# Performance work log

Hardware: AMD Instinct MI355X
Metric: run time of the kernel (lower is better)

Reference implementation:

```python
import jax, jax.numpy as jnp
import numpy as np

IMG_DIM = 512
BATCH = 32


def setup_inputs() -> dict:
    key = jax.random.key(0)
    k1, k2, k3, k4, k5 = jax.random.split(key, 5)
    N, D = BATCH, IMG_DIM
    return {
        "im1": jax.random.normal(k1, (N, 3, D, D), jnp.float32),
        "im2": jax.random.normal(k2, (N, 3, D, D), jnp.float32),
        "C": jax.random.normal(k3, (N, 2, D, D), jnp.float32),
        "M1": jax.random.uniform(k4, (N, 1, D, D), jnp.float32),
        "M2": jax.random.uniform(k5, (N, 1, D, D), jnp.float32),
    }


def _grid_q(D):
    # q[0] = row coord repeated, q[1] = col coord tiled -> [2, D*D]
    x = jnp.arange(D, dtype=jnp.float32)
    return jnp.stack([jnp.repeat(x, D), jnp.tile(x, D)], axis=0)


def _get_pixel(qi, nb_x, nb_y, imflat, D):
    # qi: [N,2,HW]; nb_x, nb_y: [N,HW] integer-valued floats; imflat: [N,3,HW]
    w = (1.0 - jnp.abs(qi[:, 0] - nb_x)) * (1.0 - jnp.abs(qi[:, 1] - nb_y))  # [N,HW]
    inds = (nb_y + D * nb_x).astype(jnp.int32)  # ind = y + D*x, detached from grads
    inds = jax.lax.stop_gradient(inds)
    px = jnp.take_along_axis(imflat, inds[:, None, :], axis=2)  # [N,3,HW]
    return w[:, None, :] * px


def _masked_rp(image, mask, qi_orig, D):
    N = image.shape[0]
    HW = D * D
    imflat = image.reshape(N, 3, HW)
    qi = jnp.clip(qi_orig, 0.001, D - 1.001)  # [N,2,HW]
    fx, fy = jnp.floor(qi[:, 0]), jnp.floor(qi[:, 1])
    cx, cy = jnp.ceil(qi[:, 0]), jnp.ceil(qi[:, 1])
    res = (_get_pixel(qi, fx, fy, imflat, D)
           + _get_pixel(qi, cx, fy, imflat, D)
           + _get_pixel(qi, fx, cy, imflat, D)
           + _get_pixel(qi, cx, cy, imflat, D))  # [N,3,HW]
    oob_loss = jnp.mean((qi_orig - qi) ** 2) / (D * D) * 0.01
    res_img = res.reshape(image.shape)
    return res_img * mask, oob_loss


def _forward(im1, im2, C, M1, M2):
    N = im1.shape[0]
    D = im1.shape[2]
    q = _grid_q(D)[None]  # [1,2,HW]
    Cflat = C.reshape(N, 2, D * D)
    a, la = _masked_rp(im1, M1, q + Cflat, D)
    b, lb = _masked_rp(im2, M2, q - Cflat, D)
    return a + b, la + lb


def reference(im1, im2, C, M1, M2):
    return _forward(im1, im2, C, M1, M2)
```

## Files before the change

kernel.cpp:

```cpp
#include <hip/hip_runtime.h>


constexpr int D    = 512;
constexpr int HW   = D * D;
constexpr int NB   = 32;
constexpr int NPIX = NB * HW;
constexpr float LOSS_SCALE = (float)(0.01 / (2.0 * (double)NPIX * (double)HW));

__device__ __forceinline__ float3 sample3(const float* __restrict__ p,
                                          float q0o, float q1o,
                                          float& oob, float& wscale)
{
    const float hi = 510.999f;
    float q0 = fminf(fmaxf(q0o, 0.001f), hi);
    float q1 = fminf(fmaxf(q1o, 0.001f), hi);
    float d0 = q0o - q0, d1 = q1o - q1;
    oob = fmaf(d0, d0, oob);
    oob = fmaf(d1, d1, oob);

    float fx = floorf(q0), fy = floorf(q1);
    float ax = q0 - fx,    ay = q1 - fy;
    wscale = ((ax == 0.0f) ? 2.0f : 1.0f) * ((ay == 0.0f) ? 2.0f : 1.0f);

    int off = (int)fy + (((int)fx) << 9);

    float r[3];
    #pragma unroll
    for (int c = 0; c < 3; ++c) {
        const float* pc = p + c * HW;
        float v00 = pc[off];
        float v01 = pc[off + 1];
        float v10 = pc[off + 512];
        float v11 = pc[off + 513];
        float top = fmaf(ay, v01 - v00, v00);
        float bot = fmaf(ay, v11 - v10, v10);
        r[c] = fmaf(ax, bot - top, top);
    }
    return make_float3(r[0], r[1], r[2]);
}

__global__ void __launch_bounds__(256)
vm_fwd(const float* __restrict__ im1, const float* __restrict__ im2,
       const float* __restrict__ C,   const float* __restrict__ M1,
       const float* __restrict__ M2,  float* __restrict__ out)
{
    const int b    = blockIdx.x;
    const int slab = ((b & 7) << 10) | (b >> 3);

    const int n   = slab >> 8;
    const int hw0 = ((slab & 255) << 10) | threadIdx.x;

    const float* Cn = C   + (size_t)n * 2 * HW;
    const float* Mp = M1  + (size_t)n * HW;
    const float* Mq = M2  + (size_t)n * HW;
    const float* p1 = im1 + (size_t)n * 3 * HW;
    const float* p2 = im2 + (size_t)n * 3 * HW;
    float* op       = out + (size_t)n * 3 * HW;

    float oob = 0.0f;

    #pragma unroll
    for (int j = 0; j < 4; ++j) {
        const int hw = hw0 + j * 256;
        const float qx = (float)(hw >> 9);
        const float qy = (float)(hw & 511);

        float c0 = __builtin_nontemporal_load(Cn + hw);
        float c1 = __builtin_nontemporal_load(Cn + HW + hw);
        float m1 = __builtin_nontemporal_load(Mp + hw);
        float m2 = __builtin_nontemporal_load(Mq + hw);

        float sA, sB;
        float3 av = sample3(p1, qx + c0, qy + c1, oob, sA);
        float3 bv = sample3(p2, qx - c0, qy - c1, oob, sB);
        float w1 = m1 * sA;
        float w2 = m2 * sB;

        __builtin_nontemporal_store(fmaf(av.x, w1, bv.x * w2), op + hw);
        __builtin_nontemporal_store(fmaf(av.y, w1, bv.y * w2), op + HW + hw);
        __builtin_nontemporal_store(fmaf(av.z, w1, bv.z * w2), op + 2 * HW + hw);
    }

    #pragma unroll
    for (int off = 32; off > 0; off >>= 1)
        oob += __shfl_down(oob, off, 64);

    __shared__ float wave_sums[4];
    int lane = threadIdx.x & 63;
    int wave = threadIdx.x >> 6;
    if (lane == 0) wave_sums[wave] = oob;
    __syncthreads();
    if (threadIdx.x == 0) {
        float s = wave_sums[0] + wave_sums[1] + wave_sums[2] + wave_sums[3];
        atomicAdd(out + (size_t)3 * NPIX, s * LOSS_SCALE);
    }
}

extern "C" void kernel_launch(void* const* d_in, const int* in_sizes, int n_in,
                              void* d_out, int out_size, void* d_ws, size_t ws_size,
                              hipStream_t stream) {
    const float* im1 = (const float*)d_in[0];
    const float* im2 = (const float*)d_in[1];
    const float* C   = (const float*)d_in[2];
    const float* M1  = (const float*)d_in[3];
    const float* M2  = (const float*)d_in[4];
    float* out = (float*)d_out;

    hipMemsetAsync(out + (size_t)3 * NPIX, 0, sizeof(float), stream);

    vm_fwd<<<8192, 256, 0, stream>>>(im1, im2, C, M1, M2, out);
}
```

Baseline: 371.8 us.

## Stage an eight-row image window in LDS for bilinear gathers

Each block copies an 8-row, 3-channel window of each source image into shared memory with vectorised loads. It then serves the bilinear gathers from LDS, falling back to global memory when a displaced sample lands outside the window. The flow and mask loads are hoisted ahead of the two image passes, and im1 and im2 are processed one after the other. The goal is to replace scattered global gathers with LDS reads, at the cost of a 48KB LDS footprint that limits occupancy, about 4x redundant window reads per block, and extra barriers.

```diff
diff --git a/kernel.cpp b/kernel.cpp
--- a/kernel.cpp
+++ b/kernel.cpp
@@ -7,9 +7,22 @@
 constexpr int NPIX = NB * HW;
 constexpr float LOSS_SCALE = (float)(0.01 / (2.0 * (double)NPIX * (double)HW));
 
-__device__ __forceinline__ float3 sample3(const float* __restrict__ p,
-                                          float q0o, float q1o,
-                                          float& oob, float& wscale)
+typedef float f4 __attribute__((ext_vector_type(4)));
+
+constexpr int WROWS = 8;
+constexpr int LDSZ  = 3 * WROWS * 512;
+
+__device__ __forceinline__ float lerp2(float v00, float v01, float v10, float v11,
+                                       float ax, float ay)
+{
+    float top = fmaf(ay, v01 - v00, v00);
+    float bot = fmaf(ay, v11 - v10, v10);
+    return fmaf(ax, bot - top, top);
+}
+
+struct Coord { float ax, ay, sc; int off; int u; bool in; };
+
+__device__ __forceinline__ Coord make_coord(float q0o, float q1o, int wlo, float& oob)
 {
     const float hi = 510.999f;
     float q0 = fminf(fmaxf(q0o, 0.001f), hi);
@@ -19,24 +32,56 @@
     oob = fmaf(d1, d1, oob);
 
     float fx = floorf(q0), fy = floorf(q1);
-    float ax = q0 - fx,    ay = q1 - fy;
-    wscale = ((ax == 0.0f) ? 2.0f : 1.0f) * ((ay == 0.0f) ? 2.0f : 1.0f);
+    Coord c;
+    c.ax = q0 - fx;
+    c.ay = q1 - fy;
+    c.sc = ((c.ax == 0.0f) ? 2.0f : 1.0f) * ((c.ay == 0.0f) ? 2.0f : 1.0f);
+    int ix = (int)fx, iy = (int)fy;
+    c.off = iy + (ix << 9);
+    c.u   = ix - wlo;
+    c.in  = (unsigned)c.u <= (unsigned)(WROWS - 2);
+    return c;
+}
 
-    int off = (int)fy + (((int)fx) << 9);
+__device__ __forceinline__ float3 sample_win(const float* __restrict__ lds,
+                                             const float* __restrict__ p,
+                                             const Coord& c)
+{
+    float r0, r1, r2;
+    if (c.in) {
+        int base = (c.u << 9) + (c.off & 511);
+        float a00 = lds[base],        a01 = lds[base + 1];
+        float a10 = lds[base + 512],  a11 = lds[base + 513];
+        r0 = lerp2(a00, a01, a10, a11, c.ax, c.ay);
+        float b00 = lds[base + 4096], b01 = lds[base + 4097];
+        float b10 = lds[base + 4608], b11 = lds[base + 4609];
+        r1 = lerp2(b00, b01, b10, b11, c.ax, c.ay);
+        float c00 = lds[base + 8192], c01 = lds[base + 8193];
+        float c10 = lds[base + 8704], c11 = lds[base + 8705];
+        r2 = lerp2(c00, c01, c10, c11, c.ax, c.ay);
+    } else {
+        const float* pc = p + c.off;
+        r0 = lerp2(pc[0],        pc[1],        pc[512],        pc[513],        c.ax, c.ay);
+        r1 = lerp2(pc[HW],       pc[HW + 1],   pc[HW + 512],   pc[HW + 513],   c.ax, c.ay);
+        r2 = lerp2(pc[2 * HW],   pc[2*HW + 1], pc[2*HW + 512], pc[2*HW + 513], c.ax, c.ay);
+    }
+    return make_float3(r0, r1, r2);
+}
 
-    float r[3];
+__device__ __forceinline__ void stage(float* __restrict__ lds,
+                                      const float* __restrict__ img,
+                                      int wlo, int tid)
+{
     #pragma unroll
-    for (int c = 0; c < 3; ++c) {
-        const float* pc = p + c * HW;
-        float v00 = pc[off];
-        float v01 = pc[off + 1];
-        float v10 = pc[off + 512];
-        float v11 = pc[off + 513];
-        float top = fmaf(ay, v01 - v00, v00);
-        float bot = fmaf(ay, v11 - v10, v10);
-        r[c] = fmaf(ax, bot - top, top);
+    for (int q = 0; q < 12; ++q) {
+        int e4    = q * 256 + tid;
+        int plane = e4 >> 7;
+        int ch    = plane >> 3;
+        int u     = plane & 7;
+        int col   = (e4 & 127) << 2;
+        f4 v = *(const f4*)(img + (size_t)ch * HW + ((wlo + u) << 9) + col);
+        *(f4*)(lds + (plane << 9) + col) = v;
     }
-    return make_float3(r[0], r[1], r[2]);
 }
 
 __global__ void __launch_bounds__(256)
@@ -44,11 +89,17 @@
        const float* __restrict__ C,   const float* __restrict__ M1,
        const float* __restrict__ M2,  float* __restrict__ out)
 {
+    __shared__ float lds[LDSZ];
+
     const int b    = blockIdx.x;
     const int slab = ((b & 7) << 10) | (b >> 3);
 
     const int n   = slab >> 8;
-    const int hw0 = ((slab & 255) << 10) | threadIdx.x;
+    const int k   = slab & 255;
+    const int r   = k << 1;
+    const int tid = threadIdx.x;
+    const int hw0 = (k << 10) | tid;
+    const int wlo = min(max(r - 3, 0), D - WROWS);
 
     const float* Cn = C   + (size_t)n * 2 * HW;
     const float* Mp = M1  + (size_t)n * HW;
@@ -57,28 +108,44 @@
     const float* p2 = im2 + (size_t)n * 3 * HW;
     float* op       = out + (size_t)n * 3 * HW;
 
+    float c0v[4], c1v[4], m1v[4], m2v[4];
+    #pragma unroll
+    for (int j = 0; j < 4; ++j) {
+        int hw = hw0 + j * 256;
+        c0v[j] = __builtin_nontemporal_load(Cn + hw);
+        c1v[j] = __builtin_nontemporal_load(Cn + HW + hw);
+        m1v[j] = __builtin_nontemporal_load(Mp + hw);
+        m2v[j] = __builtin_nontemporal_load(Mq + hw);
+    }
+
     float oob = 0.0f;
 
+    stage(lds, p1, wlo, tid);
+    __syncthreads();
+    float a0[4], a1[4], a2[4];
     #pragma unroll
     for (int j = 0; j < 4; ++j) {
-        const int hw = hw0 + j * 256;
-        const float qx = (float)(hw >> 9);
-        const float qy = (float)(hw & 511);
+        int hw = hw0 + j * 256;
+        float qx = (float)(hw >> 9), qy = (float)(hw & 511);
+        Coord cc = make_coord(qx + c0v[j], qy + c1v[j], wlo, oob);
+        float3 av = sample_win(lds, p1, cc);
+        float w1 = m1v[j] * cc.sc;
+        a0[j] = av.x * w1; a1[j] = av.y * w1; a2[j] = av.z * w1;
+    }
+    __syncthreads();
 
-        float c0 = __builtin_nontemporal_load(Cn + hw);
-        float c1 = __builtin_nontemporal_load(Cn + HW + hw);
-        float m1 = __builtin_nontemporal_load(Mp + hw);
-        float m2 = __builtin_nontemporal_load(Mq + hw);
-
-        float sA, sB;
-        float3 av = sample3(p1, qx + c0, qy + c1, oob, sA);
-        float3 bv = sample3(p2, qx - c0, qy - c1, oob, sB);
-        float w1 = m1 * sA;
-        float w2 = m2 * sB;
-
-        __builtin_nontemporal_store(fmaf(av.x, w1, bv.x * w2), op + hw);
-        __builtin_nontemporal_store(fmaf(av.y, w1, bv.y * w2), op + HW + hw);
-        __builtin_nontemporal_store(fmaf(av.z, w1, bv.z * w2), op + 2 * HW + hw);
+    stage(lds, p2, wlo, tid);
+    __syncthreads();
+    #pragma unroll
+    for (int j = 0; j < 4; ++j) {
+        int hw = hw0 + j * 256;
+        float qx = (float)(hw >> 9), qy = (float)(hw & 511);
+        Coord cc = make_coord(qx - c0v[j], qy - c1v[j], wlo, oob);
+        float3 bv = sample_win(lds, p2, cc);
+        float w2 = m2v[j] * cc.sc;
+        __builtin_nontemporal_store(fmaf(bv.x, w2, a0[j]), op + hw);
+        __builtin_nontemporal_store(fmaf(bv.y, w2, a1[j]), op + HW + hw);
+        __builtin_nontemporal_store(fmaf(bv.z, w2, a2[j]), op + 2 * HW + hw);
     }
 
     #pragma unroll
@@ -86,11 +153,11 @@
         oob += __shfl_down(oob, off, 64);
 
     __shared__ float wave_sums[4];
-    int lane = threadIdx.x & 63;
-    int wave = threadIdx.x >> 6;
+    int lane = tid & 63;
+    int wave = tid >> 6;
     if (lane == 0) wave_sums[wave] = oob;
     __syncthreads();
-    if (threadIdx.x == 0) {
+    if (tid == 0) {
         float s = wave_sums[0] + wave_sums[1] + wave_sums[2] + wave_sums[3];
         atomicAdd(out + (size_t)3 * NPIX, s * LOSS_SCALE);
     }
```

After: 340.1 us. -8.5%, faster.

## Stage an 8-row image window in LDS per channel for bilinear gathers

Applied to the files above, without the earlier changes.

Each block now cooperatively loads an 8-row window around its two output rows, for both images, into shared memory one channel at a time. Bilinear samples whose neighbours fall inside the window read from LDS, and all others fall back to global gathers. The next channel's window is prefetched into registers while the current one is consumed. This aims to replace scattered global gathers with coalesced vector loads plus LDS reads. In exchange it adds barriers, extra global traffic for the window, and branch divergence whenever the random displacement leaves the window, which with normal-distributed offsets happens for a sizable share of samples.

```diff
diff --git a/kernel.cpp b/kernel.cpp
--- a/kernel.cpp
+++ b/kernel.cpp
@@ -7,36 +7,19 @@
 constexpr int NPIX = NB * HW;
 constexpr float LOSS_SCALE = (float)(0.01 / (2.0 * (double)NPIX * (double)HW));
 
-__device__ __forceinline__ float3 sample3(const float* __restrict__ p,
-                                          float q0o, float q1o,
-                                          float& oob, float& wscale)
+typedef float f4 __attribute__((ext_vector_type(4)));
+
+constexpr int WROWS   = 8;
+constexpr int RSTRIDE = 520;
+constexpr int PLANE   = WROWS * RSTRIDE;
+constexpr int LDSZ    = 2 * PLANE;
+
+__device__ __forceinline__ float lerp2(float v00, float v01, float v10, float v11,
+                                       float ax, float ay)
 {
-    const float hi = 510.999f;
-    float q0 = fminf(fmaxf(q0o, 0.001f), hi);
-    float q1 = fminf(fmaxf(q1o, 0.001f), hi);
-    float d0 = q0o - q0, d1 = q1o - q1;
-    oob = fmaf(d0, d0, oob);
-    oob = fmaf(d1, d1, oob);
-
-    float fx = floorf(q0), fy = floorf(q1);
-    float ax = q0 - fx,    ay = q1 - fy;
-    wscale = ((ax == 0.0f) ? 2.0f : 1.0f) * ((ay == 0.0f) ? 2.0f : 1.0f);
-
-    int off = (int)fy + (((int)fx) << 9);
-
-    float r[3];
-    #pragma unroll
-    for (int c = 0; c < 3; ++c) {
-        const float* pc = p + c * HW;
-        float v00 = pc[off];
-        float v01 = pc[off + 1];
-        float v10 = pc[off + 512];
-        float v11 = pc[off + 513];
-        float top = fmaf(ay, v01 - v00, v00);
-        float bot = fmaf(ay, v11 - v10, v10);
-        r[c] = fmaf(ax, bot - top, top);
-    }
-    return make_float3(r[0], r[1], r[2]);
+    float top = fmaf(ay, v01 - v00, v00);
+    float bot = fmaf(ay, v11 - v10, v10);
+    return fmaf(ax, bot - top, top);
 }
 
 __global__ void __launch_bounds__(256)
@@ -44,11 +27,18 @@
        const float* __restrict__ C,   const float* __restrict__ M1,
        const float* __restrict__ M2,  float* __restrict__ out)
 {
+    __shared__ float lds[LDSZ];
+    __shared__ float wave_sums[4];
+
     const int b    = blockIdx.x;
     const int slab = ((b & 7) << 10) | (b >> 3);
 
     const int n   = slab >> 8;
-    const int hw0 = ((slab & 255) << 10) | threadIdx.x;
+    const int k   = slab & 255;
+    const int r   = k << 1;
+    const int tid = threadIdx.x;
+    const int hw0 = (k << 10) | tid;
+    const int wlo = min(max(r - 3, 0), D - WROWS);
 
     const float* Cn = C   + (size_t)n * 2 * HW;
     const float* Mp = M1  + (size_t)n * HW;
@@ -58,39 +48,120 @@
     float* op       = out + (size_t)n * 3 * HW;
 
     float oob = 0.0f;
+    float axA[4], ayA[4], w1v[4], axB[4], ayB[4], w2v[4];
+    int   baseA[4], offA[4], baseB[4], offB[4];
+    bool  inA[4], inB[4];
 
     #pragma unroll
     for (int j = 0; j < 4; ++j) {
         const int hw = hw0 + j * 256;
         const float qx = (float)(hw >> 9);
         const float qy = (float)(hw & 511);
-
         float c0 = __builtin_nontemporal_load(Cn + hw);
         float c1 = __builtin_nontemporal_load(Cn + HW + hw);
         float m1 = __builtin_nontemporal_load(Mp + hw);
         float m2 = __builtin_nontemporal_load(Mq + hw);
 
-        float sA, sB;
-        float3 av = sample3(p1, qx + c0, qy + c1, oob, sA);
-        float3 bv = sample3(p2, qx - c0, qy - c1, oob, sB);
-        float w1 = m1 * sA;
-        float w2 = m2 * sB;
+        const float hi = 510.999f;
+        {
+            float q0o = qx + c0, q1o = qy + c1;
+            float q0 = fminf(fmaxf(q0o, 0.001f), hi);
+            float q1 = fminf(fmaxf(q1o, 0.001f), hi);
+            float d0 = q0o - q0, d1 = q1o - q1;
+            oob = fmaf(d0, d0, oob); oob = fmaf(d1, d1, oob);
+            float fx = floorf(q0), fy = floorf(q1);
+            axA[j] = q0 - fx; ayA[j] = q1 - fy;
+            float sc = ((axA[j] == 0.0f) ? 2.0f : 1.0f) * ((ayA[j] == 0.0f) ? 2.0f : 1.0f);
+            w1v[j] = m1 * sc;
+            int ix = (int)fx, iy = (int)fy;
+            offA[j]  = iy + (ix << 9);
+            int u    = ix - wlo;
+            inA[j]   = (unsigned)u <= (unsigned)(WROWS - 2);
+            baseA[j] = u * RSTRIDE + iy;
+        }
+        {
+            float q0o = qx - c0, q1o = qy - c1;
+            float q0 = fminf(fmaxf(q0o, 0.001f), hi);
+            float q1 = fminf(fmaxf(q1o, 0.001f), hi);
+            float d0 = q0o - q0, d1 = q1o - q1;
+            oob = fmaf(d0, d0, oob); oob = fmaf(d1, d1, oob);
+            float fx = floorf(q0), fy = floorf(q1);
+            axB[j] = q0 - fx; ayB[j] = q1 - fy;
+            float sc = ((axB[j] == 0.0f) ? 2.0f : 1.0f) * ((ayB[j] == 0.0f) ? 2.0f : 1.0f);
+            w2v[j] = m2 * sc;
+            int ix = (int)fx, iy = (int)fy;
+            offB[j]  = iy + (ix << 9);
+            int u    = ix - wlo;
+            inB[j]   = (unsigned)u <= (unsigned)(WROWS - 2);
+            baseB[j] = PLANE + u * RSTRIDE + iy;
+        }
+    }
 
-        __builtin_nontemporal_store(fmaf(av.x, w1, bv.x * w2), op + hw);
-        __builtin_nontemporal_store(fmaf(av.y, w1, bv.y * w2), op + HW + hw);
-        __builtin_nontemporal_store(fmaf(av.z, w1, bv.z * w2), op + 2 * HW + hw);
+    const int su  = (tid >> 7);
+    const int sc4 = (tid & 127) << 2;
+
+    f4 pf[8];
+    #define PFLOAD(CH)                                                          \
+        _Pragma("unroll")                                                       \
+        for (int q = 0; q < 8; ++q) {                                           \
+            const float* ip = (q < 4) ? p1 : p2;                                \
+            int u = ((q & 3) << 1) + su;                                        \
+            pf[q] = *(const f4*)(ip + (size_t)(CH) * HW + ((wlo + u) << 9) + sc4); \
+        }
+    #define PFWRITE()                                                           \
+        _Pragma("unroll")                                                       \
+        for (int q = 0; q < 8; ++q) {                                           \
+            int u = ((q & 3) << 1) + su;                                        \
+            int img = (q < 4) ? 0 : 1;                                          \
+            *(f4*)(lds + img * PLANE + u * RSTRIDE + sc4) = pf[q];              \
+        }
+
+    PFLOAD(0);
+
+    #pragma unroll
+    for (int ch = 0; ch < 3; ++ch) {
+        PFWRITE();
+        __syncthreads();
+        if (ch < 2) PFLOAD(ch + 1);
+
+        const float* g1 = p1 + (size_t)ch * HW;
+        const float* g2 = p2 + (size_t)ch * HW;
+        float* oc = op + (size_t)ch * HW;
+
+        #pragma unroll
+        for (int j = 0; j < 4; ++j) {
+            float ra, rb;
+            if (inA[j]) {
+                int ba = baseA[j];
+                ra = lerp2(lds[ba], lds[ba + 1], lds[ba + RSTRIDE], lds[ba + RSTRIDE + 1],
+                           axA[j], ayA[j]);
+            } else {
+                const float* pa = g1 + offA[j];
+                ra = lerp2(pa[0], pa[1], pa[512], pa[513], axA[j], ayA[j]);
+            }
+            if (inB[j]) {
+                int bb = baseB[j];
+                rb = lerp2(lds[bb], lds[bb + 1], lds[bb + RSTRIDE], lds[bb + RSTRIDE + 1],
+                           axB[j], ayB[j]);
+            } else {
+                const float* pb = g2 + offB[j];
+                rb = lerp2(pb[0], pb[1], pb[512], pb[513], axB[j], ayB[j]);
+            }
+            __builtin_nontemporal_store(fmaf(ra, w1v[j], rb * w2v[j]),
+                                        oc + hw0 + j * 256);
+        }
+        __syncthreads();
     }
 
     #pragma unroll
     for (int off = 32; off > 0; off >>= 1)
         oob += __shfl_down(oob, off, 64);
 
-    __shared__ float wave_sums[4];
-    int lane = threadIdx.x & 63;
-    int wave = threadIdx.x >> 6;
+    int lane = tid & 63;
+    int wave = tid >> 6;
     if (lane == 0) wave_sums[wave] = oob;
     __syncthreads();
-    if (threadIdx.x == 0) {
+    if (tid == 0) {
         float s = wave_sums[0] + wave_sums[1] + wave_sums[2] + wave_sums[3];
         atomicAdd(out + (size_t)3 * NPIX, s * LOSS_SCALE);
     }
```

After: 342.8 us. 1.08x faster.
